# Kernel optimization log

Measured on AMD Instinct MI355X. Metric: run time of the kernel, lower is better.

## Reference

```python
import jax, jax.numpy as jnp
import numpy as np

B, S, D, H = 4, 2048, 512, 8
INNER = D  # assumed AttentionHead.inner_size == size (naive single-head attention)


def setup_inputs() -> dict:
    key = jax.random.key(0)
    ks = jax.random.split(key, 8)
    scale = 0.02
    return {
        "emb_input": jax.random.normal(ks[0], (B, S, D), dtype=jnp.float32),
        "Wq": jax.random.normal(ks[1], (H, D, INNER), dtype=jnp.float32) * scale,
        "bq": jnp.zeros((H, INNER), dtype=jnp.float32),
        "Wk": jax.random.normal(ks[2], (H, D, INNER), dtype=jnp.float32) * scale,
        "bk": jnp.zeros((H, INNER), dtype=jnp.float32),
        "Wv": jax.random.normal(ks[3], (H, D, INNER), dtype=jnp.float32) * scale,
        "bv": jnp.zeros((H, INNER), dtype=jnp.float32),
        "Wp": jax.random.normal(ks[4], (H * INNER, D), dtype=jnp.float32) * scale,
        "bp": jnp.zeros((D,), dtype=jnp.float32),
    }


def reference(emb_input, Wq, bq, Wk, bk, Wv, bv, Wp, bp):
    # All heads batched into one einsum instead of a Python loop over submodules.
    x = emb_input  # [B, S, D]
    q = jnp.einsum("bsd,hde->bhse", x, Wq) + bq[None, :, None, :]  # [B,H,S,E]
    k = jnp.einsum("bsd,hde->bhse", x, Wk) + bk[None, :, None, :]
    v = jnp.einsum("bsd,hde->bhse", x, Wv) + bv[None, :, None, :]
    scores = jnp.einsum("bhse,bhte->bhst", q, k) / jnp.sqrt(
        jnp.asarray(INNER, dtype=x.dtype)
    )  # [B,H,S,S]
    attn = jax.nn.softmax(scores, axis=-1)
    o = jnp.einsum("bhst,bhte->bhse", attn, v)  # [B,H,S,E]
    # concat over heads (dim=2 in torch => feature dim after per-head outputs)
    o = jnp.transpose(o, (0, 2, 1, 3)).reshape(B, S, H * INNER)
    return o @ Wp + bp  # [B, S, D]
```

## Files before the change

### kernel.cpp

```cpp
#include <hip/hip_runtime.h>


typedef short s8v __attribute__((ext_vector_type(8)));
typedef float f4v __attribute__((ext_vector_type(4)));
typedef unsigned short us;
typedef us us4v __attribute__((ext_vector_type(4)));

__device__ inline us f2b(float f) {
  union { float f; unsigned u; } v; v.f = f;
  unsigned r = v.u + 0x7FFFu + ((v.u >> 16) & 1u);
  return (us)(r >> 16);
}

__device__ inline void gld16(const us* g, us* l) {
  __builtin_amdgcn_global_load_lds(
      (const __attribute__((address_space(1))) void*)g,
      (__attribute__((address_space(3))) void*)l, 16, 0, 0);
}

template <int EPI>
__global__ __launch_bounds__(512, 2) void gemm_nt(
    const us* __restrict__ A, int lda, long long sA0, long long sA1,
    const us* __restrict__ Bm, int ldb, long long sB0, long long sB1,
    const float* __restrict__ bias, const float* __restrict__ bias2,
    const float* __restrict__ bias3,
    void* __restrict__ Cv, void* __restrict__ C2, void* __restrict__ C3,
    int ldc, long long sC0, long long sC1,
    int K, float alpha, int L, int sbits) {
  __shared__ __align__(16) us As[2][16384];
  __shared__ __align__(16) us Bs[2][16384];
  const int t = threadIdx.x;
  const int wv = t >> 6, ln = t & 63;
  const int m16 = ln & 15, quad = ln >> 4;

  const int gx = gridDim.x, gxy = gx * gridDim.y;
  const int nblk = gxy * gridDim.z;
  const int flat = blockIdx.x + gx * blockIdx.y + gxy * blockIdx.z;
  int nid = flat;
  if ((nblk & 7) == 0) nid = (flat & 7) * (nblk >> 3) + (flat >> 3);
  const int bz = nid / gxy, rem = nid % gxy;
  const int by = rem / gx, bx = rem % gx;

  const long long row0 = (long long)by * 256;
  const long long col0 = (long long)bx * 256;
  const int zo = bz >> L, zi = bz & ((1 << L) - 1);
  const us* Az = A + zo * sA0 + zi * sA1;
  const us* Bz = Bm + zo * sB0 + zi * sB1;

  int offA[4], offB[4];
#pragma unroll
  for (int j = 0; j < 4; ++j) {
    const int c = t + 512 * j;
    const int s = c >> 6, l = c & 63;
    const int mb = s >> 1, ks = s & 1, qd = (l >> 4) & 3, mm = l & 15;
    offA[j] = (int)((row0 + mb * 16 + mm) * (long long)lda + ks * 32 + qd * 8);
    offB[j] = (int)((col0 + mb * 16 + mm) * (long long)ldb + ks * 32 + qd * 8);
  }

  f4v acc[8][4];
#pragma unroll
  for (int r = 0; r < 8; ++r)
#pragma unroll
    for (int c = 0; c < 4; ++c) acc[r][c] = (f4v){0.f, 0.f, 0.f, 0.f};

  const int nk = K >> 6;
  const int wr = wv >> 2, wc = wv & 3;

#define BARR __builtin_amdgcn_s_barrier()
#define LGKM0                                              \
  do {                                                     \
    asm volatile("s_waitcnt lgkmcnt(0)" ::: "memory");     \
    __builtin_amdgcn_sched_barrier(0);                     \
  } while (0)
#define READ_A(p_)                                                           \
  _Pragma("unroll") for (int rr = 0; rr < 2; ++rr)                           \
  _Pragma("unroll") for (int ks = 0; ks < 2; ++ks)                           \
      af[rr * 2 + ks] = *(const s8v*)&As[b]                                  \
          [(((wr * 8 + (p_) * 2 + rr) * 2 + ks) * 64 + ln) * 8];
#define MFMA_Q(p_)                                                           \
  __builtin_amdgcn_s_setprio(1);                                             \
  _Pragma("unroll") for (int ks = 0; ks < 2; ++ks)                           \
  _Pragma("unroll") for (int rr = 0; rr < 2; ++rr)                           \
  _Pragma("unroll") for (int c = 0; c < 4; ++c)                              \
      acc[(p_) * 2 + rr][c] = __builtin_amdgcn_mfma_f32_16x16x32_bf16(       \
          af[rr * 2 + ks], bfr[c * 2 + ks], acc[(p_) * 2 + rr][c], 0, 0, 0); \
  __builtin_amdgcn_s_setprio(0);

#pragma unroll
  for (int j = 0; j < 4; ++j) gld16(Az + offA[j], (us*)As[0] + (t + 512 * j) * 8);
#pragma unroll
  for (int j = 0; j < 4; ++j) gld16(Bz + offB[j], (us*)Bs[0] + (t + 512 * j) * 8);
  if (nk > 1) {
#pragma unroll
    for (int j = 0; j < 4; ++j)
      gld16(Bz + offB[j] + 64, (us*)Bs[1] + (t + 512 * j) * 8);
    gld16(Az + offA[0] + 64, (us*)As[1] + t * 8);
    gld16(Az + offA[2] + 64, (us*)As[1] + (t + 1024) * 8);
    asm volatile("s_waitcnt vmcnt(6)" ::: "memory");
  } else {
    asm volatile("s_waitcnt vmcnt(0)" ::: "memory");
  }
  BARR;

  for (int kt = 0; kt < nk; ++kt) {
    const int b = kt & 1;
    s8v bfr[8], af[4];
#pragma unroll
    for (int c = 0; c < 4; ++c)
#pragma unroll
      for (int ks = 0; ks < 2; ++ks)
        bfr[c * 2 + ks] =
            *(const s8v*)&Bs[b][(((wc * 4 + c) * 2 + ks) * 64 + ln) * 8];
    READ_A(0);
    if (kt + 1 < nk) {
      const int kof = (kt + 1) << 6;
      gld16(Az + offA[1] + kof, (us*)As[b ^ 1] + (t + 512) * 8);
      gld16(Az + offA[3] + kof, (us*)As[b ^ 1] + (t + 1536) * 8);
    }
    asm volatile("s_waitcnt lgkmcnt(8)" ::: "memory");
    BARR; LGKM0; MFMA_Q(0); BARR;
    READ_A(1);
    if (kt + 2 < nk) {
      const int kof = (kt + 2) << 6;
#pragma unroll
      for (int j = 0; j < 4; ++j)
        gld16(Bz + offB[j] + kof, (us*)Bs[b] + (t + 512 * j) * 8);
    }
    BARR; LGKM0; MFMA_Q(1); BARR;
    READ_A(2);
    if (kt + 2 < nk) {
      const int kof = (kt + 2) << 6;
      gld16(Az + offA[0] + kof, (us*)As[b] + t * 8);
      gld16(Az + offA[2] + kof, (us*)As[b] + (t + 1024) * 8);
    }
    BARR; LGKM0; MFMA_Q(2); BARR;
    READ_A(3);
    BARR; LGKM0; MFMA_Q(3);
    if (kt + 2 < nk) asm volatile("s_waitcnt vmcnt(6)" ::: "memory");
    else             asm volatile("s_waitcnt vmcnt(0)" ::: "memory");
    BARR;
  }
#undef READ_A
#undef MFMA_Q
#undef BARR
#undef LGKM0

  if (EPI == 6) {
#pragma unroll
    for (int r = 0; r < 8; ++r)
#pragma unroll
      for (int c = 0; c < 4; ++c)
#pragma unroll
        for (int g = 0; g < 4; ++g)
          acc[r][c][g] = __expf(fmaf(acc[r][c][g], alpha, -4.f));
  }
#pragma unroll
  for (int r = 0; r < 8; ++r) {
    const int inRow = wr * 128 + r * 16 + quad * 4;
    const long long gr0 = row0 + inRow;
#pragma unroll
    for (int c = 0; c < 4; ++c) {
      const long long gc = col0 + wc * 64 + c * 16 + m16;
      if (EPI == 3) {
        const int which = (int)(gc >> sbits);
        const int gsec = (int)gc & ((1 << sbits) - 1);
        const int hc = gsec >> 9, e = (int)gc & 511;
        const long long slice =
            ((long long)zo * (1 << (sbits - 9)) + hc) * 1048576LL;
        if (which == 0) {
          us* C = (us*)Cv;
          const float bb = bias[gsec];
#pragma unroll
          for (int g = 0; g < 4; ++g)
            C[slice + (gr0 + g) * 512 + e] = f2b(acc[r][c][g] + bb);
        } else if (which == 1) {
          us* C = (us*)C2;
          const float bb = bias2[gsec];
#pragma unroll
          for (int g = 0; g < 4; ++g)
            C[slice + (gr0 + g) * 512 + e] = f2b(acc[r][c][g] + bb);
        } else {
          us* C = (us*)C3;
          const float bb = bias3[gsec];
          us4v pk;
#pragma unroll
          for (int g = 0; g < 4; ++g) pk[g] = f2b(acc[r][c][g] + bb);
          *(us4v*)&C[slice + (long long)e * 2048 + gr0] = pk;
        }
      } else if (EPI == 5) {
        float* C = (float*)Cv + zo * sC0;
        float* p = C + gr0 * ldc + gc;
#pragma unroll
        for (int g = 0; g < 4; ++g)
          atomicAdd(&p[(long long)g * ldc], acc[r][c][g] * alpha);
      } else if (EPI == 6) {
        us* C = (us*)Cv + zo * sC0 + zi * sC1;
#pragma unroll
        for (int g = 0; g < 4; ++g)
          C[(gr0 + g) * (long long)ldc + gc] = f2b(acc[r][c][g]);
      } else {
        us* C = (us*)Cv + zo * sC0 + zi * sC1;
        const float* lrow = (const float*)C2 + (long long)bz * 2048;
#pragma unroll
        for (int g = 0; g < 4; ++g) {
          const float inv = 1.f / lrow[gr0 + g];
          C[(gr0 + g) * (long long)ldc + gc] = f2b(acc[r][c][g] * inv);
        }
      }
    }
    if (EPI == 6) {
      float* lsum = (float*)C2 + (long long)bz * 2048;
#pragma unroll
      for (int g = 0; g < 4; ++g) {
        float s = acc[r][0][g] + acc[r][1][g] + acc[r][2][g] + acc[r][3][g];
        s += __shfl_xor(s, 1, 64);
        s += __shfl_xor(s, 2, 64);
        s += __shfl_xor(s, 4, 64);
        s += __shfl_xor(s, 8, 64);
        if (m16 == 0) atomicAdd(&lsum[gr0 + g], s);
      }
    }
  }
}

__global__ __launch_bounds__(256) void conv_bf16(const float* __restrict__ in,
                                                 us* __restrict__ out, int n4) {
  const int i = blockIdx.x * 256 + threadIdx.x;
  if (i < n4) {
    const float4 f = ((const float4*)in)[i];
    us4v o;
    o[0] = f2b(f.x); o[1] = f2b(f.y); o[2] = f2b(f.z); o[3] = f2b(f.w);
    ((us4v*)out)[i] = o;
  }
}

__global__ __launch_bounds__(256) void conv_transpose(const float* __restrict__ in,
                                                      us* __restrict__ out,
                                                      int R, int C, int Lc,
                                                      int mask, long long sChunk) {
  __shared__ float tile[32][33];
  const int tx = threadIdx.x & 31, ty = threadIdx.x >> 5;
  const int z = blockIdx.z;
  const long long zi = (long long)z * R * C;
  us* dst = out + (long long)(z >> Lc) * sChunk + (long long)(z & mask) * R * C;
  const int r0 = blockIdx.y * 32, c0 = blockIdx.x * 32;
#pragma unroll
  for (int j = 0; j < 4; ++j)
    tile[ty + 8 * j][tx] = in[zi + (long long)(r0 + ty + 8 * j) * C + c0 + tx];
  __syncthreads();
#pragma unroll
  for (int j = 0; j < 4; ++j)
    dst[(long long)(c0 + ty + 8 * j) * R + r0 + tx] = f2b(tile[tx][ty + 8 * j]);
}

__global__ __launch_bounds__(256) void init_out_kernel(float* __restrict__ out,
                                                       const float* __restrict__ bp,
                                                       int total,
                                                       float* __restrict__ lz,
                                                       int lcnt) {
  const int i = blockIdx.x * 256 + threadIdx.x;
  if (i < total) out[i] = bp[i & 511];
  else if (i < total + lcnt) lz[i - total] = 0.f;
}

extern "C" void kernel_launch(void* const* d_in, const int* in_sizes, int n_in,
                              void* d_out, int out_size, void* d_ws, size_t ws_size,
                              hipStream_t stream) {
  constexpr int Bb = 4, S = 2048, D = 512, H = 8, E = 512, HE = 4096;
  const float* x  = (const float*)d_in[0];
  const float* Wq = (const float*)d_in[1];
  const float* bq = (const float*)d_in[2];
  const float* Wk = (const float*)d_in[3];
  const float* bk = (const float*)d_in[4];
  const float* Wv = (const float*)d_in[5];
  const float* bv = (const float*)d_in[6];
  const float* Wp = (const float*)d_in[7];
  const float* bp = (const float*)d_in[8];
  float* out = (float*)d_out;

  const long long SE = (long long)S * E, SS = (long long)S * S;
  const long long SD = (long long)S * D, ED = (long long)E * D;

  us* xh  = (us*)d_ws;
  us* W3  = xh + 4194304;
  us* WpT = W3 + 6291456;
  us* dyn = WpT + 2097152;

  const size_t fixedB = (size_t)(4194304 + 6291456 + 2097152) * 2;
  const size_t lB = (size_t)H * Bb * S * 4;
  int HC = 8;
  while (HC > 1) {
    const size_t need = fixedB + lB +
        (size_t)HC * (3 * (size_t)Bb * SE + (size_t)Bb * SS) * 2;
    if (need <= ws_size) break;
    HC >>= 1;
  }
  const int Lh = (HC == 8) ? 3 : (HC == 4) ? 2 : (HC == 2) ? 1 : 0;
  const int BHC = Bb * HC;
  const int sbits = 9 + Lh;

  us* qh = dyn;
  us* kh = qh + (size_t)BHC * SE;
  us* vT = kh + (size_t)BHC * SE;
  us* sc = vT + (size_t)BHC * SE;
  float* lb = (float*)(sc + (size_t)BHC * SS);
  us* oh = qh;

  const dim3 tb(256), tg(512);
  const int lcnt = H * Bb * S;
  init_out_kernel<<<dim3((Bb * S * D + lcnt + 255) / 256), tb, 0, stream>>>(
      out, bp, Bb * S * D, lb, lcnt);
  conv_bf16<<<dim3(4194304 / 4 / 256), tb, 0, stream>>>(x, xh, 4194304 / 4);
  const long long sChunk = 3LL * HC * ED;
  conv_transpose<<<dim3(16, 16, H), tb, 0, stream>>>(Wq, W3, D, E, Lh, HC - 1, sChunk);
  conv_transpose<<<dim3(16, 16, H), tb, 0, stream>>>(Wk, W3 + HC * ED, D, E, Lh, HC - 1, sChunk);
  conv_transpose<<<dim3(16, 16, H), tb, 0, stream>>>(Wv, W3 + 2 * HC * ED, D, E, Lh, HC - 1, sChunk);
  conv_transpose<<<dim3(16, 128, 1), tb, 0, stream>>>(Wp, WpT, HE, D, 0, 0, 0);

  const float aS = 0.044194173824159216f;
  const dim3 gQKV(3 * HC * E / 256, 8, Bb);
  const dim3 gS(8, 8, BHC);
  const dim3 gPV(2, 8, BHC);
  const dim3 gOP(2, 8, BHC);

  for (int c = 0; c < H / HC; ++c) {
    const int h0 = c * HC;
    float* lc = lb + (long long)c * BHC * S;
    gemm_nt<3><<<gQKV, tg, 0, stream>>>(
        xh, D, SD, 0, W3 + c * sChunk, D, 0, 0,
        bq + h0 * E, bk + h0 * E, bv + h0 * E,
        qh, kh, vT, 512, 0, SE, D, 1.f, 0, sbits);
    gemm_nt<6><<<gS, tg, 0, stream>>>(
        qh, E, (long long)HC * SE, SE, kh, E, (long long)HC * SE, SE,
        nullptr, nullptr, nullptr, sc, lc, nullptr,
        S, (long long)HC * SS, SS, E, aS, Lh, 0);
    gemm_nt<7><<<gPV, tg, 0, stream>>>(
        sc, S, (long long)HC * SS, SS, vT, S, (long long)HC * SE, SE,
        nullptr, nullptr, nullptr, oh, lc, nullptr,
        HC * E, (long long)S * HC * E, E, S, 1.f, Lh, 0);
    gemm_nt<5><<<gOP, tg, 0, stream>>>(
        oh, HC * E, (long long)S * HC * E, 512,
        WpT + (long long)h0 * E, HE, 0, 512,
        nullptr, nullptr, nullptr, out, nullptr, nullptr,
        D, SD, 0, 512, 1.f, Lh, 0);
  }
}
```

Before: 935.2 us.

## Fuse QK^T, exp and PV into one flash-style attention kernel

Replaces the separate score GEMM (which wrote bf16 exp-scores and atomically accumulated row sums) and the PV GEMM with one fused kernel. It keeps a 128-row Q tile in registers, streams K and V^T tiles through a double-buffered LDS ring with global_load_lds, computes exp scores per tile, passes P through LDS and accumulates O in registers. This removes the S×S score buffer round-trip through HBM and the row-sum atomics. In exchange it uses a fixed exp offset instead of a running max and holds a large register-resident O accumulator, which may limit occupancy.

```diff
diff --git a/kernel.cpp b/kernel.cpp
--- a/kernel.cpp
+++ b/kernel.cpp
@@ -16,6 +16,148 @@
   __builtin_amdgcn_global_load_lds(
       (const __attribute__((address_space(1))) void*)g,
       (__attribute__((address_space(3))) void*)l, 16, 0, 0);
+}
+
+__global__ __launch_bounds__(512, 2) void attn_fused(
+    const us* __restrict__ Q, const us* __restrict__ Kh,
+    const us* __restrict__ Vt, us* __restrict__ O,
+    int Lh, float alpha) {
+  constexpr int S = 2048, E = 512;
+  constexpr int NCH = (S / 128) * 8;
+  __shared__ __align__(16) us ring[2][16384];
+  __shared__ __align__(16) us Ps[8][2176];
+  const int t = threadIdx.x, w = t >> 6, ln = t & 63;
+  const int m16 = ln & 15, quad = ln >> 4;
+
+  const int gx = gridDim.x;
+  const int nblk = gx * gridDim.y;
+  const int flat = blockIdx.x + gx * blockIdx.y;
+  int nid = flat;
+  if ((nblk & 7) == 0) nid = (flat & 7) * (nblk >> 3) + (flat >> 3);
+  const int qt = nid % gx, zh = nid / gx;
+
+  const long long zoff = (long long)zh * S * E;
+  const us* Qz = Q + zoff;
+  const us* Kz = Kh + zoff;
+  const us* Vz = Vt + zoff;
+  const int q0 = qt * 128;
+
+  s8v Qf[16];
+  {
+    const us* qrow = Qz + (long long)(q0 + 16 * w + m16) * E + quad * 8;
+#pragma unroll
+    for (int kq = 0; kq < 16; ++kq) Qf[kq] = *(const s8v*)(qrow + kq * 32);
+  }
+
+  f4v accO[4][8];
+#pragma unroll
+  for (int e = 0; e < 4; ++e)
+#pragma unroll
+    for (int nb = 0; nb < 8; ++nb) accO[e][nb] = (f4v){0.f, 0.f, 0.f, 0.f};
+  float la[4] = {0.f, 0.f, 0.f, 0.f};
+
+#define STAGE(g_)                                                            \
+  {                                                                          \
+    const int tau_ = (g_) >> 3, sub_ = (g_) & 7;                             \
+    us* dst_ = (us*)ring[(g_) & 1];                                          \
+    _Pragma("unroll") for (int j = 0; j < 4; ++j) {                          \
+      const int c_ = t + 512 * j;                                            \
+      const int s_ = c_ >> 6, l_ = c_ & 63;                                  \
+      const int nbm_ = ((s_ >> 2) * 16 + (l_ & 15));                         \
+      const int kk_ = (s_ & 3) * 32 + (l_ >> 4) * 8;                         \
+      const us* src_ = (sub_ < 4)                                            \
+          ? Kz + (long long)(tau_ * 128 + nbm_) * E + sub_ * 128 + kk_       \
+          : Vz + (long long)((sub_ - 4) * 128 + nbm_) * S + tau_ * 128 + kk_;\
+      gld16(src_, dst_ + c_ * 8);                                            \
+    }                                                                        \
+  }
+
+  STAGE(0);
+  STAGE(1);
+
+  for (int tau = 0; tau < S / 128; ++tau) {
+    f4v accS[8];
+#pragma unroll
+    for (int nb = 0; nb < 8; ++nb) accS[nb] = (f4v){0.f, 0.f, 0.f, 0.f};
+    s8v pa[4];
+#pragma unroll
+    for (int ph = 0; ph < 8; ++ph) {
+      const int g = tau * 8 + ph;
+      if (g + 1 < NCH) asm volatile("s_waitcnt vmcnt(4)" ::: "memory");
+      else             asm volatile("s_waitcnt vmcnt(0)" ::: "memory");
+      __builtin_amdgcn_s_barrier();
+      const us* rb = (const us*)ring[g & 1];
+      __builtin_amdgcn_s_setprio(1);
+#pragma unroll
+      for (int ks = 0; ks < 4; ++ks) {
+#pragma unroll
+        for (int h = 0; h < 2; ++h) {
+          s8v bf[4];
+#pragma unroll
+          for (int nb = 0; nb < 4; ++nb)
+            bf[nb] = *(const s8v*)&rb[(((h * 4 + nb) * 4 + ks) * 64 + ln) * 8];
+          if (ph < 4) {
+#pragma unroll
+            for (int nb = 0; nb < 4; ++nb)
+              accS[h * 4 + nb] = __builtin_amdgcn_mfma_f32_16x16x32_bf16(
+                  Qf[ph * 4 + ks], bf[nb], accS[h * 4 + nb], 0, 0, 0);
+          } else {
+#pragma unroll
+            for (int nb = 0; nb < 4; ++nb)
+              accO[ph - 4][h * 4 + nb] = __builtin_amdgcn_mfma_f32_16x16x32_bf16(
+                  pa[ks], bf[nb], accO[ph - 4][h * 4 + nb], 0, 0, 0);
+          }
+        }
+      }
+      __builtin_amdgcn_s_setprio(0);
+      __builtin_amdgcn_s_barrier();
+      if (g + 2 < NCH) STAGE(g + 2);
+      if (ph == 3) {
+        us* pw = &Ps[w][0];
+#pragma unroll
+        for (int nb = 0; nb < 8; ++nb)
+#pragma unroll
+          for (int gg = 0; gg < 4; ++gg) {
+            accS[nb][gg] = __expf(fmaf(accS[nb][gg], alpha, -4.f));
+            pw[(quad * 4 + gg) * 136 + nb * 16 + m16] = f2b(accS[nb][gg]);
+          }
+#pragma unroll
+        for (int gg = 0; gg < 4; ++gg) {
+          float s = 0.f;
+#pragma unroll
+          for (int nb = 0; nb < 8; ++nb) s += accS[nb][gg];
+          s += __shfl_xor(s, 1, 64);
+          s += __shfl_xor(s, 2, 64);
+          s += __shfl_xor(s, 4, 64);
+          s += __shfl_xor(s, 8, 64);
+          la[gg] += s;
+        }
+        asm volatile("s_waitcnt lgkmcnt(0)" ::: "memory");
+        __builtin_amdgcn_sched_barrier(0);
+#pragma unroll
+        for (int kp = 0; kp < 4; ++kp)
+          pa[kp] = *(const s8v*)&pw[m16 * 136 + kp * 32 + quad * 8];
+      }
+    }
+  }
+#undef STAGE
+
+  float inv[4];
+#pragma unroll
+  for (int gg = 0; gg < 4; ++gg) inv[gg] = 1.f / la[gg];
+  const int b = zh >> Lh, hc = zh & ((1 << Lh) - 1);
+  const int HCE = E << Lh;
+  us* Ob = O + (long long)b * S * HCE + (long long)hc * E;
+#pragma unroll
+  for (int ec = 0; ec < 4; ++ec)
+#pragma unroll
+    for (int nb = 0; nb < 8; ++nb) {
+      const int ecol = ec * 128 + nb * 16 + m16;
+#pragma unroll
+      for (int gg = 0; gg < 4; ++gg)
+        Ob[(long long)(q0 + 16 * w + quad * 4 + gg) * HCE + ecol] =
+            f2b(accO[ec][nb][gg] * inv[gg]);
+    }
 }
 
 template <int EPI>
@@ -145,15 +287,6 @@
 #undef BARR
 #undef LGKM0
 
-  if (EPI == 6) {
-#pragma unroll
-    for (int r = 0; r < 8; ++r)
-#pragma unroll
-      for (int c = 0; c < 4; ++c)
-#pragma unroll
-        for (int g = 0; g < 4; ++g)
-          acc[r][c][g] = __expf(fmaf(acc[r][c][g], alpha, -4.f));
-  }
 #pragma unroll
   for (int r = 0; r < 8; ++r) {
     const int inRow = wr * 128 + r * 16 + quad * 4;
@@ -187,37 +320,12 @@
           for (int g = 0; g < 4; ++g) pk[g] = f2b(acc[r][c][g] + bb);
           *(us4v*)&C[slice + (long long)e * 2048 + gr0] = pk;
         }
-      } else if (EPI == 5) {
+      } else {
         float* C = (float*)Cv + zo * sC0;
         float* p = C + gr0 * ldc + gc;
 #pragma unroll
         for (int g = 0; g < 4; ++g)
           atomicAdd(&p[(long long)g * ldc], acc[r][c][g] * alpha);
-      } else if (EPI == 6) {
-        us* C = (us*)Cv + zo * sC0 + zi * sC1;
-#pragma unroll
-        for (int g = 0; g < 4; ++g)
-          C[(gr0 + g) * (long long)ldc + gc] = f2b(acc[r][c][g]);
-      } else {
-        us* C = (us*)Cv + zo * sC0 + zi * sC1;
-        const float* lrow = (const float*)C2 + (long long)bz * 2048;
-#pragma unroll
-        for (int g = 0; g < 4; ++g) {
-          const float inv = 1.f / lrow[gr0 + g];
-          C[(gr0 + g) * (long long)ldc + gc] = f2b(acc[r][c][g] * inv);
-        }
-      }
-    }
-    if (EPI == 6) {
-      float* lsum = (float*)C2 + (long long)bz * 2048;
-#pragma unroll
-      for (int g = 0; g < 4; ++g) {
-        float s = acc[r][0][g] + acc[r][1][g] + acc[r][2][g] + acc[r][3][g];
-        s += __shfl_xor(s, 1, 64);
-        s += __shfl_xor(s, 2, 64);
-        s += __shfl_xor(s, 4, 64);
-        s += __shfl_xor(s, 8, 64);
-        if (m16 == 0) atomicAdd(&lsum[gr0 + g], s);
       }
     }
   }
@@ -255,12 +363,9 @@
 
 __global__ __launch_bounds__(256) void init_out_kernel(float* __restrict__ out,
                                                        const float* __restrict__ bp,
-                                                       int total,
-                                                       float* __restrict__ lz,
-                                                       int lcnt) {
+                                                       int total) {
   const int i = blockIdx.x * 256 + threadIdx.x;
   if (i < total) out[i] = bp[i & 511];
-  else if (i < total + lcnt) lz[i - total] = 0.f;
 }
 
 extern "C" void kernel_launch(void* const* d_in, const int* in_sizes, int n_in,
@@ -278,7 +383,7 @@
   const float* bp = (const float*)d_in[8];
   float* out = (float*)d_out;
 
-  const long long SE = (long long)S * E, SS = (long long)S * S;
+  const long long SE = (long long)S * E;
   const long long SD = (long long)S * D, ED = (long long)E * D;
 
   us* xh  = (us*)d_ws;
@@ -287,11 +392,9 @@
   us* dyn = WpT + 2097152;
 
   const size_t fixedB = (size_t)(4194304 + 6291456 + 2097152) * 2;
-  const size_t lB = (size_t)H * Bb * S * 4;
   int HC = 8;
   while (HC > 1) {
-    const size_t need = fixedB + lB +
-        (size_t)HC * (3 * (size_t)Bb * SE + (size_t)Bb * SS) * 2;
+    const size_t need = fixedB + (size_t)4 * HC * Bb * SE * 2;
     if (need <= ws_size) break;
     HC >>= 1;
   }
@@ -302,14 +405,11 @@
   us* qh = dyn;
   us* kh = qh + (size_t)BHC * SE;
   us* vT = kh + (size_t)BHC * SE;
-  us* sc = vT + (size_t)BHC * SE;
-  float* lb = (float*)(sc + (size_t)BHC * SS);
-  us* oh = qh;
+  us* oh = vT + (size_t)BHC * SE;
 
   const dim3 tb(256), tg(512);
-  const int lcnt = H * Bb * S;
-  init_out_kernel<<<dim3((Bb * S * D + lcnt + 255) / 256), tb, 0, stream>>>(
-      out, bp, Bb * S * D, lb, lcnt);
+  init_out_kernel<<<dim3((Bb * S * D + 255) / 256), tb, 0, stream>>>(
+      out, bp, Bb * S * D);
   conv_bf16<<<dim3(4194304 / 4 / 256), tb, 0, stream>>>(x, xh, 4194304 / 4);
   const long long sChunk = 3LL * HC * ED;
   conv_transpose<<<dim3(16, 16, H), tb, 0, stream>>>(Wq, W3, D, E, Lh, HC - 1, sChunk);
@@ -319,25 +419,16 @@
 
   const float aS = 0.044194173824159216f;
   const dim3 gQKV(3 * HC * E / 256, 8, Bb);
-  const dim3 gS(8, 8, BHC);
-  const dim3 gPV(2, 8, BHC);
+  const dim3 gAT(S / 128, BHC);
   const dim3 gOP(2, 8, BHC);
 
   for (int c = 0; c < H / HC; ++c) {
     const int h0 = c * HC;
-    float* lc = lb + (long long)c * BHC * S;
     gemm_nt<3><<<gQKV, tg, 0, stream>>>(
         xh, D, SD, 0, W3 + c * sChunk, D, 0, 0,
         bq + h0 * E, bk + h0 * E, bv + h0 * E,
         qh, kh, vT, 512, 0, SE, D, 1.f, 0, sbits);
-    gemm_nt<6><<<gS, tg, 0, stream>>>(
-        qh, E, (long long)HC * SE, SE, kh, E, (long long)HC * SE, SE,
-        nullptr, nullptr, nullptr, sc, lc, nullptr,
-        S, (long long)HC * SS, SS, E, aS, Lh, 0);
-    gemm_nt<7><<<gPV, tg, 0, stream>>>(
-        sc, S, (long long)HC * SS, SS, vT, S, (long long)HC * SE, SE,
-        nullptr, nullptr, nullptr, oh, lc, nullptr,
-        HC * E, (long long)S * HC * E, E, S, 1.f, Lh, 0);
+    attn_fused<<<gAT, tg, 0, stream>>>(qh, kh, vT, oh, Lh, aS);
     gemm_nt<5><<<gOP, tg, 0, stream>>>(
         oh, HC * E, (long long)S * HC * E, 512,
         WpT + (long long)h0 * E, HE, 0, 512,
```

New measurement: 1.040 ms. 11.2% more time.

## Halve GEMM K-tile to 32 and permute LDS row-block layout

Applied to the files above, without the earlier changes.

The bf16 GEMM K-step per tile drops from 64 to 32, which halves the LDS buffers to 8192 elements each. The loop is restructured into two phases of 16 MFMAs each, with global-to-LDS loads and vmcnt waits rebalanced to match. A PERM swizzle remaps the 16-row block index in LDS, apparently to reduce bank conflicts or improve load locality. The smaller LDS footprint could allow more occupancy, but the K-loop runs twice as many iterations, so there is more barrier and sync overhead per FLOP.

```diff
diff --git a/kernel.cpp b/kernel.cpp
--- a/kernel.cpp
+++ b/kernel.cpp
@@ -17,6 +17,8 @@
       (const __attribute__((address_space(1))) void*)g,
       (__attribute__((address_space(3))) void*)l, 16, 0, 0);
 }
+
+#define PERM(s_) (((s_) & 3) | (((s_) & 4) << 1) | (((s_) & 8) >> 1))
 
 template <int EPI>
 __global__ __launch_bounds__(512, 2) void gemm_nt(
@@ -27,8 +29,8 @@
     void* __restrict__ Cv, void* __restrict__ C2, void* __restrict__ C3,
     int ldc, long long sC0, long long sC1,
     int K, float alpha, int L, int sbits) {
-  __shared__ __align__(16) us As[2][16384];
-  __shared__ __align__(16) us Bs[2][16384];
+  __shared__ __align__(16) us As[2][8192];
+  __shared__ __align__(16) us Bs[2][8192];
   const int t = threadIdx.x;
   const int wv = t >> 6, ln = t & 63;
   const int m16 = ln & 15, quad = ln >> 4;
@@ -47,14 +49,15 @@
   const us* Az = A + zo * sA0 + zi * sA1;
   const us* Bz = Bm + zo * sB0 + zi * sB1;
 
-  int offA[4], offB[4];
-#pragma unroll
-  for (int j = 0; j < 4; ++j) {
+  int offA[2], offB[2];
+#pragma unroll
+  for (int j = 0; j < 2; ++j) {
     const int c = t + 512 * j;
-    const int s = c >> 6, l = c & 63;
-    const int mb = s >> 1, ks = s & 1, qd = (l >> 4) & 3, mm = l & 15;
-    offA[j] = (int)((row0 + mb * 16 + mm) * (long long)lda + ks * 32 + qd * 8);
-    offB[j] = (int)((col0 + mb * 16 + mm) * (long long)ldb + ks * 32 + qd * 8);
+    const int s = c >> 6;
+    const int sp = PERM(s);
+    const int mm = c & 15, qd = (c >> 4) & 3;
+    offA[j] = (int)((row0 + sp * 16 + mm) * (long long)lda + qd * 8);
+    offB[j] = (int)((col0 + sp * 16 + mm) * (long long)ldb + qd * 8);
   }
 
   f4v acc[8][4];
@@ -63,7 +66,7 @@
 #pragma unroll
     for (int c = 0; c < 4; ++c) acc[r][c] = (f4v){0.f, 0.f, 0.f, 0.f};
 
-  const int nk = K >> 6;
+  const int nk = K >> 5;
   const int wr = wv >> 2, wc = wv & 3;
 
 #define BARR __builtin_amdgcn_s_barrier()
@@ -72,31 +75,23 @@
     asm volatile("s_waitcnt lgkmcnt(0)" ::: "memory");     \
     __builtin_amdgcn_sched_barrier(0);                     \
   } while (0)
-#define READ_A(p_)                                                           \
-  _Pragma("unroll") for (int rr = 0; rr < 2; ++rr)                           \
-  _Pragma("unroll") for (int ks = 0; ks < 2; ++ks)                           \
-      af[rr * 2 + ks] = *(const s8v*)&As[b]                                  \
-          [(((wr * 8 + (p_) * 2 + rr) * 2 + ks) * 64 + ln) * 8];
-#define MFMA_Q(p_)                                                           \
+#define MFMA16(r0_)                                                          \
   __builtin_amdgcn_s_setprio(1);                                             \
-  _Pragma("unroll") for (int ks = 0; ks < 2; ++ks)                           \
-  _Pragma("unroll") for (int rr = 0; rr < 2; ++rr)                           \
-  _Pragma("unroll") for (int c = 0; c < 4; ++c)                              \
-      acc[(p_) * 2 + rr][c] = __builtin_amdgcn_mfma_f32_16x16x32_bf16(       \
-          af[rr * 2 + ks], bfr[c * 2 + ks], acc[(p_) * 2 + rr][c], 0, 0, 0); \
+  _Pragma("unroll") for (int rr = 0; rr < 4; ++rr)                           \
+  _Pragma("unroll") for (int cc = 0; cc < 4; ++cc)                           \
+      acc[(r0_) + rr][cc] = __builtin_amdgcn_mfma_f32_16x16x32_bf16(         \
+          af[rr], bfr[cc], acc[(r0_) + rr][cc], 0, 0, 0);                    \
   __builtin_amdgcn_s_setprio(0);
 
-#pragma unroll
-  for (int j = 0; j < 4; ++j) gld16(Az + offA[j], (us*)As[0] + (t + 512 * j) * 8);
-#pragma unroll
-  for (int j = 0; j < 4; ++j) gld16(Bz + offB[j], (us*)Bs[0] + (t + 512 * j) * 8);
+  gld16(Bz + offB[0], (us*)Bs[0] + t * 8);
+  gld16(Bz + offB[1], (us*)Bs[0] + (t + 512) * 8);
+  gld16(Az + offA[0], (us*)As[0] + t * 8);
+  gld16(Az + offA[1], (us*)As[0] + (t + 512) * 8);
   if (nk > 1) {
-#pragma unroll
-    for (int j = 0; j < 4; ++j)
-      gld16(Bz + offB[j] + 64, (us*)Bs[1] + (t + 512 * j) * 8);
-    gld16(Az + offA[0] + 64, (us*)As[1] + t * 8);
-    gld16(Az + offA[2] + 64, (us*)As[1] + (t + 1024) * 8);
-    asm volatile("s_waitcnt vmcnt(6)" ::: "memory");
+    gld16(Bz + offB[0] + 32, (us*)Bs[1] + t * 8);
+    gld16(Bz + offB[1] + 32, (us*)Bs[1] + (t + 512) * 8);
+    gld16(Az + offA[0] + 32, (us*)As[1] + t * 8);
+    asm volatile("s_waitcnt vmcnt(3)" ::: "memory");
   } else {
     asm volatile("s_waitcnt vmcnt(0)" ::: "memory");
   }
@@ -104,44 +99,31 @@
 
   for (int kt = 0; kt < nk; ++kt) {
     const int b = kt & 1;
-    s8v bfr[8], af[4];
-#pragma unroll
-    for (int c = 0; c < 4; ++c)
-#pragma unroll
-      for (int ks = 0; ks < 2; ++ks)
-        bfr[c * 2 + ks] =
-            *(const s8v*)&Bs[b][(((wc * 4 + c) * 2 + ks) * 64 + ln) * 8];
-    READ_A(0);
-    if (kt + 1 < nk) {
-      const int kof = (kt + 1) << 6;
-      gld16(Az + offA[1] + kof, (us*)As[b ^ 1] + (t + 512) * 8);
-      gld16(Az + offA[3] + kof, (us*)As[b ^ 1] + (t + 1536) * 8);
+    s8v bfr[4], af[4];
+#pragma unroll
+    for (int cc = 0; cc < 4; ++cc)
+      bfr[cc] = *(const s8v*)&Bs[b][(PERM(wc * 4 + cc) * 64 + ln) * 8];
+#pragma unroll
+    for (int rr = 0; rr < 4; ++rr)
+      af[rr] = *(const s8v*)&As[b][(PERM(wr * 8 + rr) * 64 + ln) * 8];
+    if (kt + 1 < nk)
+      gld16(Az + offA[1] + ((kt + 1) << 5), (us*)As[b ^ 1] + (t + 512) * 8);
+    BARR; LGKM0; MFMA16(0); BARR;
+#pragma unroll
+    for (int rr = 0; rr < 4; ++rr)
+      af[rr] = *(const s8v*)&As[b][(PERM(wr * 8 + 4 + rr) * 64 + ln) * 8];
+    if (kt + 2 < nk) {
+      const int kof = (kt + 2) << 5;
+      gld16(Bz + offB[0] + kof, (us*)Bs[b] + t * 8);
+      gld16(Bz + offB[1] + kof, (us*)Bs[b] + (t + 512) * 8);
+      gld16(Az + offA[0] + kof, (us*)As[b] + t * 8);
     }
-    asm volatile("s_waitcnt lgkmcnt(8)" ::: "memory");
-    BARR; LGKM0; MFMA_Q(0); BARR;
-    READ_A(1);
-    if (kt + 2 < nk) {
-      const int kof = (kt + 2) << 6;
-#pragma unroll
-      for (int j = 0; j < 4; ++j)
-        gld16(Bz + offB[j] + kof, (us*)Bs[b] + (t + 512 * j) * 8);
-    }
-    BARR; LGKM0; MFMA_Q(1); BARR;
-    READ_A(2);
-    if (kt + 2 < nk) {
-      const int kof = (kt + 2) << 6;
-      gld16(Az + offA[0] + kof, (us*)As[b] + t * 8);
-      gld16(Az + offA[2] + kof, (us*)As[b] + (t + 1024) * 8);
-    }
-    BARR; LGKM0; MFMA_Q(2); BARR;
-    READ_A(3);
-    BARR; LGKM0; MFMA_Q(3);
-    if (kt + 2 < nk) asm volatile("s_waitcnt vmcnt(6)" ::: "memory");
+    BARR; LGKM0; MFMA16(4);
+    if (kt + 2 < nk) asm volatile("s_waitcnt vmcnt(3)" ::: "memory");
     else             asm volatile("s_waitcnt vmcnt(0)" ::: "memory");
     BARR;
   }
-#undef READ_A
-#undef MFMA_Q
+#undef MFMA16
 #undef BARR
 #undef LGKM0
 
```

Measured after the change: 911.8 us. 1.03x faster.
